# Kernel tuning notes

Hardware: AMD Instinct MI355X
Metric: run time of the kernel (lower is better)

The kernel has to match this reference:

```python
import jax, jax.numpy as jnp
import numpy as np

QMAX = 127.0  # int8 symmetric range


def _fake_quant(x, axes):
    """AQT-style int8 symmetric fake-quant over contraction axes.

    Returns quantized integer values (stored as f32) and per-channel scales
    (keepdims over `axes`).
    """
    absmax = jnp.max(jnp.abs(x), axis=axes, keepdims=True)
    scale = jnp.where(absmax > 0, absmax / QMAX, jnp.ones_like(absmax))
    q = jnp.clip(jnp.round(x / scale), -QMAX, QMAX)
    return q, scale


def setup_inputs() -> dict:
    key = jax.random.key(0)
    k1, k2 = jax.random.split(key)
    lhs = jax.random.normal(k1, (4, 16384, 512), dtype=jnp.float32)
    rhs = jax.random.normal(k2, (512, 512), dtype=jnp.float32)
    return {"lhs": lhs, "rhs": rhs}


def reference(lhs, rhs):
    # dimension_numbers = (((2,), (0,)), ((), ())) -- Dense-style contraction.
    # Quantize each operand symmetrically to int8 along its contraction axis.
    lhs_q, lhs_scale = _fake_quant(lhs, axes=(2,))   # lhs_q: [B,S,D], scale: [B,S,1]
    rhs_q, rhs_scale = _fake_quant(rhs, axes=(0,))   # rhs_q: [D,F], scale: [1,F]
    # Integer-valued matmul (accumulation exact in f32 for these magnitudes),
    # then dequantize with the outer product of scales.
    acc = jnp.einsum('bsd,df->bsf', lhs_q, rhs_q)    # [B,S,F]
    return acc * lhs_scale * rhs_scale               # broadcast [B,S,1]*[1,F]
```

## Files before the change

### kernel.cpp

```cpp
#include <hip/hip_runtime.h>
#include <hip/hip_bf16.h>
#include <stdint.h>

#define QMAX 127.0f

typedef __attribute__((ext_vector_type(4))) int   i32x4;
typedef __attribute__((ext_vector_type(2))) int   i32x2;
typedef __attribute__((ext_vector_type(4))) float f32x4v;

typedef __attribute__((address_space(1))) const void GVoid;
typedef __attribute__((address_space(3))) void LVoid;

__device__ inline int quant_i(float x, float inv) {
    float q = rintf(x * inv);
    q = fminf(fmaxf(q, -QMAX), QMAX);
    return (int)q;
}

__device__ inline uint32_t pack4(f32x4v v, float inv) {
    return (uint32_t)(quant_i(v.x, inv) & 255)
         | ((uint32_t)(quant_i(v.y, inv) & 255) << 8)
         | ((uint32_t)(quant_i(v.z, inv) & 255) << 16)
         | ((uint32_t)(quant_i(v.w, inv) & 255) << 24);
}

__device__ inline float amax8(f32x4v a, f32x4v b) {
    return fmaxf(fmaxf(fmaxf(fabsf(a.x), fabsf(a.y)), fmaxf(fabsf(a.z), fabsf(a.w))),
                 fmaxf(fmaxf(fabsf(b.x), fabsf(b.y)), fmaxf(fabsf(b.z), fabsf(b.w))));
}

__global__ __launch_bounds__(256, 8) void quant_kernel(const float* __restrict__ lhs,
                                                       const float* __restrict__ rhs,
                                                       int8_t* __restrict__ Aq,
                                                       int8_t* __restrict__ Bt,
                                                       float* __restrict__ lscale,
                                                       float* __restrict__ rscale,
                                                       int nLhs) {
    const int lane = threadIdx.x & 63;
    const int wave = threadIdx.x >> 6;
    const int bid  = blockIdx.x;

    if (bid >= nLhs) {
        const int f = (bid - nLhs) * 4 + wave;
        float v[8];
        float amax = 0.f;
#pragma unroll
        for (int i = 0; i < 8; ++i) {
            v[i] = rhs[(size_t)(lane + 64 * i) * 512 + f];
            amax = fmaxf(amax, fabsf(v[i]));
        }
#pragma unroll
        for (int m = 1; m <= 32; m <<= 1)
            amax = fmaxf(amax, __shfl_xor(amax, m, 64));
        const float inv = amax > 0.f ? QMAX / amax : 0.f;
        if (lane == 0) rscale[f] = amax > 0.f ? amax * (1.0f / QMAX) : 1.0f;
#pragma unroll
        for (int i = 0; i < 8; ++i)
            Bt[(size_t)f * 512 + lane + 64 * i] = (int8_t)quant_i(v[i], inv);
        return;
    }

    const int row0 = bid * 32 + wave * 8;
    const float* rp = lhs + (size_t)row0 * 512 + lane * 8;
    int8_t* op = Aq + (size_t)row0 * 512 + lane * 8;
#pragma unroll
    for (int r = 0; r < 8; r += 2) {
        const f32x4v a0 = __builtin_nontemporal_load((const f32x4v*)(rp + (size_t)r * 512));
        const f32x4v b0 = __builtin_nontemporal_load((const f32x4v*)(rp + (size_t)r * 512 + 4));
        const f32x4v a1 = __builtin_nontemporal_load((const f32x4v*)(rp + (size_t)(r + 1) * 512));
        const f32x4v b1 = __builtin_nontemporal_load((const f32x4v*)(rp + (size_t)(r + 1) * 512 + 4));
        float m0 = amax8(a0, b0);
        float m1 = amax8(a1, b1);
#pragma unroll
        for (int m = 1; m <= 32; m <<= 1) {
            m0 = fmaxf(m0, __shfl_xor(m0, m, 64));
            m1 = fmaxf(m1, __shfl_xor(m1, m, 64));
        }
        const float inv0 = m0 > 0.f ? QMAX / m0 : 0.f;
        const float inv1 = m1 > 0.f ? QMAX / m1 : 0.f;
        if (lane == 0) {
            lscale[row0 + r]     = m0 > 0.f ? m0 * (1.0f / QMAX) : 1.0f;
            lscale[row0 + r + 1] = m1 > 0.f ? m1 * (1.0f / QMAX) : 1.0f;
        }
        i32x2 p0, p1;
        p0.x = (int)pack4(a0, inv0); p0.y = (int)pack4(b0, inv0);
        p1.x = (int)pack4(a1, inv1); p1.y = (int)pack4(b1, inv1);
        *(i32x2*)(op + (size_t)r * 512)       = p0;
        *(i32x2*)(op + (size_t)(r + 1) * 512) = p1;
    }
}

__global__ __launch_bounds__(256, 2) void gemm_kernel(const int8_t* __restrict__ Aq,
                                                      const int8_t* __restrict__ Bt,
                                                      const float* __restrict__ lscale,
                                                      const float* __restrict__ rscale,
                                                      float* __restrict__ out) {
    __shared__ int8_t lds[65536];

    const int tid  = threadIdx.x;
    const int lane = tid & 63;
    const int wave = tid >> 6;
    const int wr   = wave >> 1;
    const int wc   = wave & 1;

    const int g   = blockIdx.x;
    const int xcd = g & 7;
    const int j   = g >> 3;
    const int m0  = (xcd * 64 + (j >> 2)) * 128;
    const int n0  = (j & 3) * 128;

    i32x4 acc[4][4];
#pragma unroll
    for (int i = 0; i < 4; ++i)
#pragma unroll
        for (int jj = 0; jj < 4; ++jj)
            acc[i][jj] = (i32x4){0, 0, 0, 0};

    const int lane15 = lane & 15;
    const int laneHi = lane >> 4;

#define STAGE(KT, BUF)                                                              \
    {                                                                               \
        _Pragma("unroll")                                                           \
        for (int c = 0; c < 4; ++c) {                                               \
            const int chunk = (c * 4 + wave) * 1024;                                \
            const int d     = chunk + lane * 16;                                    \
            const int row   = d >> 7;                                               \
            const int srck  = (d & 127) ^ ((row & 7) << 4);                         \
            const int8_t* sA = Aq + (size_t)(m0 + row) * 512 + (KT) + srck;         \
            __builtin_amdgcn_global_load_lds((GVoid*)sA, (LVoid*)(lds + (BUF) + chunk), 16, 0, 0); \
            const int8_t* sB = Bt + (size_t)(n0 + row) * 512 + (KT) + srck;         \
            __builtin_amdgcn_global_load_lds((GVoid*)sB, (LVoid*)(lds + (BUF) + 16384 + chunk), 16, 0, 0); \
        }                                                                           \
    }

    STAGE(0, 0)

#pragma unroll
    for (int t = 0; t < 4; ++t) {
        const int buf = (t & 1) * 32768;
        if (t < 3) {
            STAGE((t + 1) * 128, ((t + 1) & 1) * 32768)
            asm volatile("s_waitcnt vmcnt(8)" ::: "memory");
        } else {
            asm volatile("s_waitcnt vmcnt(0)" ::: "memory");
        }
        __builtin_amdgcn_s_barrier();
        __builtin_amdgcn_sched_barrier(0);

        i32x4 af[4][2], bf[4][2];
#pragma unroll
        for (int mi = 0; mi < 4; ++mi) {
            const int row = wr * 64 + mi * 16 + lane15;
            const int sw  = (row & 7) << 4;
#pragma unroll
            for (int kk = 0; kk < 2; ++kk) {
                const int kb = kk * 64 + laneHi * 16;
                af[mi][kk] = *(const i32x4*)(lds + buf + row * 128 + (kb ^ sw));
            }
        }
#pragma unroll
        for (int ni = 0; ni < 4; ++ni) {
            const int col = wc * 64 + ni * 16 + lane15;
            const int sw  = (col & 7) << 4;
#pragma unroll
            for (int kk = 0; kk < 2; ++kk) {
                const int kb = kk * 64 + laneHi * 16;
                bf[ni][kk] = *(const i32x4*)(lds + buf + 16384 + col * 128 + (kb ^ sw));
            }
        }
#pragma unroll
        for (int kk = 0; kk < 2; ++kk)
#pragma unroll
            for (int mi = 0; mi < 4; ++mi)
#pragma unroll
                for (int ni = 0; ni < 4; ++ni)
                    acc[mi][ni] = __builtin_amdgcn_mfma_i32_16x16x64_i8(
                        af[mi][kk], bf[ni][kk], acc[mi][ni], 0, 0, 0);

        if (t < 3) __builtin_amdgcn_s_barrier();
    }
#undef STAGE

    float rs[4];
#pragma unroll
    for (int ni = 0; ni < 4; ++ni)
        rs[ni] = rscale[n0 + wc * 64 + ni * 16 + lane15];
    const int rg = laneHi * 4;
#pragma unroll
    for (int mi = 0; mi < 4; ++mi) {
#pragma unroll
        for (int r = 0; r < 4; ++r) {
            const int grow = m0 + wr * 64 + mi * 16 + rg + r;
            const float ls = lscale[grow];
            float* op = out + (size_t)grow * 512 + n0 + wc * 64;
#pragma unroll
            for (int ni = 0; ni < 4; ++ni)
                op[ni * 16 + lane15] = (float)acc[mi][ni][r] * ls * rs[ni];
        }
    }
}

extern "C" void kernel_launch(void* const* d_in, const int* in_sizes, int n_in,
                              void* d_out, int out_size, void* d_ws, size_t ws_size,
                              hipStream_t stream) {
    const float* lhs = (const float*)d_in[0];
    const float* rhs = (const float*)d_in[1];
    float* out = (float*)d_out;

    char* ws = (char*)d_ws;
    int8_t* Bt    = (int8_t*)ws;
    float* rscale = (float*)(ws + 262144);
    float* lscale = (float*)(ws + 266240);
    int8_t* Aq    = (int8_t*)(ws + 1048576);

    const int rows = in_sizes[0] / 512;
    const int nLhs = rows / 32;

    quant_kernel<<<nLhs + 128, 256, 0, stream>>>(lhs, rhs, Aq, Bt, lscale, rscale, nLhs);
    gemm_kernel<<<(rows / 128) * 4, 256, 0, stream>>>(Aq, Bt, lscale, rscale, out);
}
```

Before: 70.93 us.

## Pre-swizzle quantized B into MFMA fragment layout and load it directly from global

The quant kernel now writes the quantized rhs in a fragment-ready layout, so each lane's 16-byte MFMA B operand sits contiguously. The GEMM drops B staging through LDS and loads B fragments straight from global/L2 into registers, halving LDS use per block to 32 KB. Occupancy bounds rise from 2 to 3 blocks per CU. The trade-off is that B loads are now issued synchronously at each k-step without prefetch, which may expose L2 latency. B is small, though, and should stay resident in cache.

```diff
diff --git a/kernel.cpp b/kernel.cpp
--- a/kernel.cpp
+++ b/kernel.cpp
@@ -32,7 +32,7 @@
 __global__ __launch_bounds__(256, 8) void quant_kernel(const float* __restrict__ lhs,
                                                        const float* __restrict__ rhs,
                                                        int8_t* __restrict__ Aq,
-                                                       int8_t* __restrict__ Bt,
+                                                       int8_t* __restrict__ Btf,
                                                        float* __restrict__ lscale,
                                                        float* __restrict__ rscale,
                                                        int nLhs) {
@@ -54,9 +54,11 @@
             amax = fmaxf(amax, __shfl_xor(amax, m, 64));
         const float inv = amax > 0.f ? QMAX / amax : 0.f;
         if (lane == 0) rscale[f] = amax > 0.f ? amax * (1.0f / QMAX) : 1.0f;
+        const int laneHi = lane >> 4, lane15 = lane & 15;
+        const int fbase = (f >> 4) * 1024 + (f & 15) * 16 + laneHi * 256 + lane15;
 #pragma unroll
         for (int i = 0; i < 8; ++i)
-            Bt[(size_t)f * 512 + lane + 64 * i] = (int8_t)quant_i(v[i], inv);
+            Btf[i * 32768 + fbase] = (int8_t)quant_i(v[i], inv);
         return;
     }
 
@@ -90,12 +92,12 @@
     }
 }
 
-__global__ __launch_bounds__(256, 2) void gemm_kernel(const int8_t* __restrict__ Aq,
-                                                      const int8_t* __restrict__ Bt,
+__global__ __launch_bounds__(256, 3) void gemm_kernel(const int8_t* __restrict__ Aq,
+                                                      const int8_t* __restrict__ Btf,
                                                       const float* __restrict__ lscale,
                                                       const float* __restrict__ rscale,
                                                       float* __restrict__ out) {
-    __shared__ int8_t lds[65536];
+    __shared__ int8_t lds[32768];
 
     const int tid  = threadIdx.x;
     const int lane = tid & 63;
@@ -118,8 +120,9 @@
 
     const int lane15 = lane & 15;
     const int laneHi = lane >> 4;
-
-#define STAGE(KT, BUF)                                                              \
+    const int8_t* bbase = Btf + (size_t)(n0 >> 4) * 1024 + (size_t)wc * 4096 + lane * 16;
+
+#define STAGE_A(KT, BUF)                                                            \
     {                                                                               \
         _Pragma("unroll")                                                           \
         for (int c = 0; c < 4; ++c) {                                               \
@@ -129,19 +132,17 @@
             const int srck  = (d & 127) ^ ((row & 7) << 4);                         \
             const int8_t* sA = Aq + (size_t)(m0 + row) * 512 + (KT) + srck;         \
             __builtin_amdgcn_global_load_lds((GVoid*)sA, (LVoid*)(lds + (BUF) + chunk), 16, 0, 0); \
-            const int8_t* sB = Bt + (size_t)(n0 + row) * 512 + (KT) + srck;         \
-            __builtin_amdgcn_global_load_lds((GVoid*)sB, (LVoid*)(lds + (BUF) + 16384 + chunk), 16, 0, 0); \
         }                                                                           \
     }
 
-    STAGE(0, 0)
+    STAGE_A(0, 0)
 
 #pragma unroll
     for (int t = 0; t < 4; ++t) {
-        const int buf = (t & 1) * 32768;
+        const int buf = (t & 1) * 16384;
         if (t < 3) {
-            STAGE((t + 1) * 128, ((t + 1) & 1) * 32768)
-            asm volatile("s_waitcnt vmcnt(8)" ::: "memory");
+            STAGE_A((t + 1) * 128, ((t + 1) & 1) * 16384)
+            asm volatile("s_waitcnt vmcnt(4)" ::: "memory");
         } else {
             asm volatile("s_waitcnt vmcnt(0)" ::: "memory");
         }
@@ -149,6 +150,11 @@
         __builtin_amdgcn_sched_barrier(0);
 
         i32x4 af[4][2], bf[4][2];
+#pragma unroll
+        for (int ni = 0; ni < 4; ++ni)
+#pragma unroll
+            for (int kk = 0; kk < 2; ++kk)
+                bf[ni][kk] = *(const i32x4*)(bbase + (size_t)(t * 2 + kk) * 32768 + ni * 1024);
 #pragma unroll
         for (int mi = 0; mi < 4; ++mi) {
             const int row = wr * 64 + mi * 16 + lane15;
@@ -160,16 +166,6 @@
             }
         }
 #pragma unroll
-        for (int ni = 0; ni < 4; ++ni) {
-            const int col = wc * 64 + ni * 16 + lane15;
-            const int sw  = (col & 7) << 4;
-#pragma unroll
-            for (int kk = 0; kk < 2; ++kk) {
-                const int kb = kk * 64 + laneHi * 16;
-                bf[ni][kk] = *(const i32x4*)(lds + buf + 16384 + col * 128 + (kb ^ sw));
-            }
-        }
-#pragma unroll
         for (int kk = 0; kk < 2; ++kk)
 #pragma unroll
             for (int mi = 0; mi < 4; ++mi)
@@ -180,7 +176,7 @@
 
         if (t < 3) __builtin_amdgcn_s_barrier();
     }
-#undef STAGE
+#undef STAGE_A
 
     float rs[4];
 #pragma unroll
@@ -209,7 +205,7 @@
     float* out = (float*)d_out;
 
     char* ws = (char*)d_ws;
-    int8_t* Bt    = (int8_t*)ws;
+    int8_t* Btf   = (int8_t*)ws;
     float* rscale = (float*)(ws + 262144);
     float* lscale = (float*)(ws + 266240);
     int8_t* Aq    = (int8_t*)(ws + 1048576);
@@ -217,6 +213,6 @@
     const int rows = in_sizes[0] / 512;
     const int nLhs = rows / 32;
 
-    quant_kernel<<<nLhs + 128, 256, 0, stream>>>(lhs, rhs, Aq, Bt, lscale, rscale, nLhs);
-    gemm_kernel<<<(rows / 128) * 4, 256, 0, stream>>>(Aq, Bt, lscale, rscale, out);
-}
+    quant_kernel<<<nLhs + 128, 256, 0, stream>>>(lhs, rhs, Aq, Btf, lscale, rscale, nLhs);
+    gemm_kernel<<<(rows / 128) * 4, 256, 0, stream>>>(Aq, Btf, lscale, rscale, out);
+}
```

New measurement: 72.13 us. Within noise of the previous version (+1.7%).
